# Optimization experiments

Measured on AMD Instinct MI355X. Metric: run time of the kernel, lower is better.

## Reference

```python
import jax, jax.numpy as jnp
import numpy as np

NUM_EDGE_TYPES = 38
NUM_NODE_TYPES = 4
HIDDEN = 64
HOPS = 4
N_NODES = 100_000
N_EDGES = 1_600_000


def setup_inputs() -> dict:
    key = jax.random.key(0)
    ks = jax.random.split(key, 7)
    in_dim = NUM_EDGE_TYPES + 2 * NUM_NODE_TYPES  # 46
    return {
        "edge_index": jax.random.randint(ks[0], (2, N_EDGES), 0, N_NODES),
        "edge_type": jax.random.randint(ks[1], (N_EDGES,), 0, NUM_EDGE_TYPES),
        "node_type": jax.random.randint(ks[2], (N_NODES,), 0, NUM_NODE_TYPES),
        "W1": jax.random.normal(ks[3], (in_dim, HIDDEN), dtype=jnp.float32) * 0.1,
        "b1": jax.random.normal(ks[4], (HIDDEN,), dtype=jnp.float32) * 0.1,
        "W2": jax.random.normal(ks[5], (HIDDEN, 1), dtype=jnp.float32) * 0.1,
        "b2": jax.random.normal(ks[6], (1,), dtype=jnp.float32) * 0.1,
    }


def reference(edge_index, edge_type, node_type, W1, b1, W2, b2):
    src, dst = edge_index[0], edge_index[1]  # PyG: x_j = x[edge_index[0]], aggregate at edge_index[1]
    head_type = node_type[src]
    tail_type = node_type[dst]
    # Linear over concat of three one-hots == sum of three gathered weight rows + bias.
    h = (W1[edge_type]
         + W1[NUM_EDGE_TYPES + head_type]
         + W1[NUM_EDGE_TYPES + NUM_NODE_TYPES + tail_type]
         + b1)                                   # [E, HIDDEN]
    h = jax.nn.gelu(h)
    edge_emb = jax.nn.sigmoid(h @ W2 + b2)       # [E, 1]

    num_nodes = node_type.shape[0]
    aggr = jnp.zeros((num_nodes, 1), dtype=edge_emb.dtype)
    for _ in range(HOPS):
        msg = aggr[src] + edge_emb               # gather + add, [E, 1]
        aggr = jax.ops.segment_sum(msg, dst, num_segments=num_nodes)  # scatter-add
    return aggr
```

## Files before the change

### kernel.cpp

```cpp
#include <hip/hip_runtime.h>

#define NUM_EDGE_TYPES 38
#define NUM_NODE_TYPES 4
#define HIDDEN 64
#define TABLE_SIZE (NUM_EDGE_TYPES * NUM_NODE_TYPES * NUM_NODE_TYPES)
#define SRC_BITS 17
#define SRC_MASK ((1 << SRC_BITS) - 1)
#define BSHIFT 8
#define BNODES 256
#define MAXB 512
#define CHUNK 4096
#define PB 512
#define HB 1024

__global__ void partition_kernel(const int* __restrict__ src, const int* __restrict__ dst,
                                 const int* __restrict__ etype, int* __restrict__ cursor,
                                 int* __restrict__ pack, int E, int nbk, int cap) {
    __shared__ int hist[MAXB];
    __shared__ int locCur[MAXB];
    for (int i = threadIdx.x; i < nbk; i += PB) hist[i] = 0;
    __syncthreads();
    int start = blockIdx.x * CHUNK;
    int end = min(start + CHUNK, E);
    if (end - start == CHUNK) {
        int j = start + threadIdx.x;
        int d[8], s[8], et[8], slot[8];
#pragma unroll
        for (int k = 0; k < 8; ++k) d[k] = dst[j + k * PB];
#pragma unroll
        for (int k = 0; k < 8; ++k) atomicAdd(&hist[d[k] >> BSHIFT], 1);
        __syncthreads();
        for (int i = threadIdx.x; i < nbk; i += PB) {
            int h = hist[i];
            locCur[i] = h ? i * cap + atomicAdd(&cursor[i], h) : 0;
        }
        __syncthreads();
#pragma unroll
        for (int k = 0; k < 8; ++k) s[k] = src[j + k * PB];
#pragma unroll
        for (int k = 0; k < 8; ++k) et[k] = etype[j + k * PB];
#pragma unroll
        for (int k = 0; k < 8; ++k) slot[k] = atomicAdd(&locCur[d[k] >> BSHIFT], 1);
#pragma unroll
        for (int k = 0; k < 8; ++k)
            pack[slot[k]] = (et[k] << (SRC_BITS + 8)) | ((d[k] & (BNODES - 1)) << SRC_BITS) | s[k];
    } else {
        for (int j = start + threadIdx.x; j < end; j += PB)
            atomicAdd(&hist[dst[j] >> BSHIFT], 1);
        __syncthreads();
        for (int i = threadIdx.x; i < nbk; i += PB) {
            int h = hist[i];
            locCur[i] = h ? i * cap + atomicAdd(&cursor[i], h) : 0;
        }
        __syncthreads();
        for (int j = start + threadIdx.x; j < end; j += PB) {
            int d = dst[j];
            int slot = atomicAdd(&locCur[d >> BSHIFT], 1);
            pack[slot] = (etype[j] << (SRC_BITS + 8)) | ((d & (BNODES - 1)) << SRC_BITS) | src[j];
        }
    }
}

__global__ void base_kernel(const int* __restrict__ pack, const int* __restrict__ cursor,
                            const int* __restrict__ ntype,
                            const float* __restrict__ W1, const float* __restrict__ b1,
                            const float* __restrict__ W2, const float* __restrict__ b2,
                            float* __restrict__ base, int N, int cap) {
    __shared__ float bins[BNODES];
    __shared__ float tbl[TABLE_SIZE];
    __shared__ unsigned char ntLoc[BNODES];
    int b = blockIdx.x;
    int node0 = b << BSHIFT;
    if (threadIdx.x < TABLE_SIZE) {
        int i = threadIdx.x;
        int et = i >> 4, ht = (i >> 2) & 3, tt = i & 3;
        const float* r0 = W1 + et * HIDDEN;
        const float* r1 = W1 + (NUM_EDGE_TYPES + ht) * HIDDEN;
        const float* r2 = W1 + (NUM_EDGE_TYPES + NUM_NODE_TYPES + tt) * HIDDEN;
        float acc = b2[0];
#pragma unroll 8
        for (int k = 0; k < HIDDEN; ++k) {
            float h = r0[k] + r1[k] + r2[k] + b1[k];
            float u = 0.7978845608028654f * (h + 0.044715f * h * h * h);
            float g = 0.5f * h * (1.0f + tanhf(u));
            acc += g * W2[k];
        }
        tbl[i] = 1.0f / (1.0f + expf(-acc));
    }
    if (threadIdx.x < BNODES) {
        bins[threadIdx.x] = 0.0f;
        int n = node0 + threadIdx.x;
        ntLoc[threadIdx.x] = (n < N) ? (unsigned char)ntype[n] : 0;
    }
    __syncthreads();
    int st = b * cap;
    int end = st + cursor[b];
    int j = st + threadIdx.x;
    for (; j + 3 * HB < end; j += 4 * HB) {
        int p0 = pack[j], p1 = pack[j + HB], p2 = pack[j + 2 * HB], p3 = pack[j + 3 * HB];
        int n0 = ntype[p0 & SRC_MASK], n1 = ntype[p1 & SRC_MASK];
        int n2 = ntype[p2 & SRC_MASK], n3 = ntype[p3 & SRC_MASK];
        int dl0 = (p0 >> SRC_BITS) & (BNODES - 1), dl1 = (p1 >> SRC_BITS) & (BNODES - 1);
        int dl2 = (p2 >> SRC_BITS) & (BNODES - 1), dl3 = (p3 >> SRC_BITS) & (BNODES - 1);
        atomicAdd(&bins[dl0], tbl[((((unsigned)p0) >> (SRC_BITS + 8)) << 4) | (n0 << 2) | ntLoc[dl0]]);
        atomicAdd(&bins[dl1], tbl[((((unsigned)p1) >> (SRC_BITS + 8)) << 4) | (n1 << 2) | ntLoc[dl1]]);
        atomicAdd(&bins[dl2], tbl[((((unsigned)p2) >> (SRC_BITS + 8)) << 4) | (n2 << 2) | ntLoc[dl2]]);
        atomicAdd(&bins[dl3], tbl[((((unsigned)p3) >> (SRC_BITS + 8)) << 4) | (n3 << 2) | ntLoc[dl3]]);
    }
    for (; j < end; j += HB) {
        int p = pack[j];
        int dl = (p >> SRC_BITS) & (BNODES - 1);
        int idx = ((((unsigned)p) >> (SRC_BITS + 8)) << 4) | (ntype[p & SRC_MASK] << 2) | ntLoc[dl];
        atomicAdd(&bins[dl], tbl[idx]);
    }
    __syncthreads();
    if (threadIdx.x < BNODES) {
        int n = node0 + threadIdx.x;
        if (n < N) base[n] = bins[threadIdx.x];
    }
}

__global__ void hop_kernel(const int* __restrict__ pack, const int* __restrict__ cursor,
                           const float* __restrict__ base, const float* __restrict__ prev,
                           float* __restrict__ out, int N, int cap) {
    __shared__ float bins[BNODES];
    int b = blockIdx.x;
    if (threadIdx.x < BNODES) bins[threadIdx.x] = 0.0f;
    __syncthreads();
    int st = b * cap;
    int end = st + cursor[b];
    int j = st + threadIdx.x;
    for (; j + 3 * HB < end; j += 4 * HB) {
        int p0 = pack[j], p1 = pack[j + HB], p2 = pack[j + 2 * HB], p3 = pack[j + 3 * HB];
        float v0 = prev[p0 & SRC_MASK], v1 = prev[p1 & SRC_MASK];
        float v2 = prev[p2 & SRC_MASK], v3 = prev[p3 & SRC_MASK];
        atomicAdd(&bins[(p0 >> SRC_BITS) & (BNODES - 1)], v0);
        atomicAdd(&bins[(p1 >> SRC_BITS) & (BNODES - 1)], v1);
        atomicAdd(&bins[(p2 >> SRC_BITS) & (BNODES - 1)], v2);
        atomicAdd(&bins[(p3 >> SRC_BITS) & (BNODES - 1)], v3);
    }
    for (; j < end; j += HB) {
        int p = pack[j];
        atomicAdd(&bins[(p >> SRC_BITS) & (BNODES - 1)], prev[p & SRC_MASK]);
    }
    __syncthreads();
    if (threadIdx.x < BNODES) {
        int n = (b << BSHIFT) + threadIdx.x;
        if (n < N) out[n] = base[n] + bins[threadIdx.x];
    }
}

__global__ void table_kernel(const float* __restrict__ W1, const float* __restrict__ b1,
                             const float* __restrict__ W2, const float* __restrict__ b2,
                             float* __restrict__ table) {
    int i = blockIdx.x * blockDim.x + threadIdx.x;
    if (i >= TABLE_SIZE) return;
    int et = i >> 4, ht = (i >> 2) & 3, tt = i & 3;
    const float* r0 = W1 + et * HIDDEN;
    const float* r1 = W1 + (NUM_EDGE_TYPES + ht) * HIDDEN;
    const float* r2 = W1 + (NUM_EDGE_TYPES + NUM_NODE_TYPES + tt) * HIDDEN;
    float acc = b2[0];
#pragma unroll 8
    for (int k = 0; k < HIDDEN; ++k) {
        float h = r0[k] + r1[k] + r2[k] + b1[k];
        float u = 0.7978845608028654f * (h + 0.044715f * h * h * h);
        float g = 0.5f * h * (1.0f + tanhf(u));
        acc += g * W2[k];
    }
    table[i] = 1.0f / (1.0f + expf(-acc));
}

__global__ void edge_base_kernel(const int* __restrict__ src, const int* __restrict__ dst,
                                 const int* __restrict__ etype, const int* __restrict__ ntype,
                                 const float* __restrict__ table, float* __restrict__ base, int E) {
    __shared__ float tbl[TABLE_SIZE];
    for (int i = threadIdx.x; i < TABLE_SIZE; i += blockDim.x) tbl[i] = table[i];
    __syncthreads();
    int e = blockIdx.x * blockDim.x + threadIdx.x;
    if (e >= E) return;
    int s = src[e];
    int d = dst[e];
    int idx = (etype[e] << 4) | (ntype[s] << 2) | ntype[d];
    atomicAdd(base + d, tbl[idx]);
}

__global__ void copy_kernel(const float* __restrict__ in, float* __restrict__ out, int N) {
    int i = blockIdx.x * blockDim.x + threadIdx.x;
    if (i < N) out[i] = in[i];
}

__global__ void edge_hop_kernel(const int* __restrict__ src, const int* __restrict__ dst,
                                const float* __restrict__ prev, float* __restrict__ next, int E) {
    int e = blockIdx.x * blockDim.x + threadIdx.x;
    if (e >= E) return;
    atomicAdd(next + dst[e], prev[src[e]]);
}

extern "C" void kernel_launch(void* const* d_in, const int* in_sizes, int n_in,
                              void* d_out, int out_size, void* d_ws, size_t ws_size,
                              hipStream_t stream) {
    const int* edge_index = (const int*)d_in[0];
    const int* etype      = (const int*)d_in[1];
    const int* ntype      = (const int*)d_in[2];
    const float* W1       = (const float*)d_in[3];
    const float* b1       = (const float*)d_in[4];
    const float* W2       = (const float*)d_in[5];
    const float* b2       = (const float*)d_in[6];

    const int E = in_sizes[1];
    const int N = in_sizes[2];
    const int* src = edge_index;
    const int* dst = edge_index + E;
    float* out = (float*)d_out;

    const int nbk = (N + BNODES - 1) >> BSHIFT;
    const int nChunks = (E + CHUNK - 1) / CHUNK;

    int cap = ((E / (nbk > 0 ? nbk : 1)) * 3 / 2 + 255) & ~255;
    if (cap < 512) cap = 512;
    size_t packElems = (size_t)nbk * cap;

    size_t need = (packElems + MAXB + (size_t)3 * N) * 4 + 256;

    if (ws_size >= need && nbk <= MAXB) {
        int* pack   = (int*)d_ws;
        int* cursor = pack + packElems;
        float* base = (float*)(cursor + MAXB);
        float* bufA = base + N;
        float* bufB = bufA + N;

        hipMemsetAsync(cursor, 0, (size_t)nbk * sizeof(int), stream);

        partition_kernel<<<nChunks, PB, 0, stream>>>(src, dst, etype, cursor, pack, E, nbk, cap);
        base_kernel<<<nbk, HB, 0, stream>>>(pack, cursor, ntype, W1, b1, W2, b2, base, N, cap);
        hop_kernel<<<nbk, HB, 0, stream>>>(pack, cursor, base, base, bufA, N, cap);
        hop_kernel<<<nbk, HB, 0, stream>>>(pack, cursor, base, bufA, bufB, N, cap);
        hop_kernel<<<nbk, HB, 0, stream>>>(pack, cursor, base, bufB, out, N, cap);
    } else {
        float* table = (float*)d_ws;
        float* base  = table + 1024;
        float* bufA  = base + N;
        float* bufB  = bufA + N;
        const int eb = (E + 255) / 256;
        const int nb = (N + 255) / 256;

        hipMemsetAsync(base, 0, (size_t)N * sizeof(float), stream);
        table_kernel<<<(TABLE_SIZE + 255) / 256, 256, 0, stream>>>(W1, b1, W2, b2, table);

        edge_base_kernel<<<eb, 256, 0, stream>>>(src, dst, etype, ntype, table, base, E);
        copy_kernel<<<nb, 256, 0, stream>>>(base, bufA, N);
        edge_hop_kernel<<<eb, 256, 0, stream>>>(src, dst, base, bufA, E);
        copy_kernel<<<nb, 256, 0, stream>>>(base, bufB, N);
        edge_hop_kernel<<<eb, 256, 0, stream>>>(src, dst, bufA, bufB, E);
        copy_kernel<<<nb, 256, 0, stream>>>(base, out, N);
        edge_hop_kernel<<<eb, 256, 0, stream>>>(src, dst, bufB, out, E);
    }
}
```

Baseline: 167.5 us.

## Sort bucket edges by destination into CSR and replace LDS atomics with segmented sums

The base kernel now counting-sorts each bucket's packed edges by local destination node in shared memory, writes the sorted edges back, and stores per-node offsets. The hop kernels then read these CSR segments with four lanes per node and reduce through shuffles, so the shared-memory float atomics on every hop go away. This adds a sort pass and extra writes in the base kernel, and the fast path now requires cap to fit in a fixed shared buffer. Work per node is uneven and each four-lane group does strided small reads, which may hurt coalescing.

```diff
diff --git a/kernel.cpp b/kernel.cpp
--- a/kernel.cpp
+++ b/kernel.cpp
@@ -12,6 +12,7 @@
 #define CHUNK 4096
 #define PB 512
 #define HB 1024
+#define CAPC 6144
 
 __global__ void partition_kernel(const int* __restrict__ src, const int* __restrict__ dst,
                                  const int* __restrict__ etype, int* __restrict__ cursor,
@@ -61,18 +62,26 @@
     }
 }
 
-__global__ void base_kernel(const int* __restrict__ pack, const int* __restrict__ cursor,
-                            const int* __restrict__ ntype,
-                            const float* __restrict__ W1, const float* __restrict__ b1,
-                            const float* __restrict__ W2, const float* __restrict__ b2,
-                            float* __restrict__ base, int N, int cap) {
-    __shared__ float bins[BNODES];
+__global__ void sort_base_kernel(int* __restrict__ pack, const int* __restrict__ cursor,
+                                 const int* __restrict__ ntype,
+                                 const float* __restrict__ W1, const float* __restrict__ b1,
+                                 const float* __restrict__ W2, const float* __restrict__ b2,
+                                 float* __restrict__ base, int* __restrict__ nodeOffG,
+                                 int N, int cap) {
+    __shared__ int sortedL[CAPC];
     __shared__ float tbl[TABLE_SIZE];
+    __shared__ int nodeCnt[BNODES];
+    __shared__ int nodeOff[BNODES + 1];
     __shared__ unsigned char ntLoc[BNODES];
     int b = blockIdx.x;
     int node0 = b << BSHIFT;
-    if (threadIdx.x < TABLE_SIZE) {
-        int i = threadIdx.x;
+    int tid = threadIdx.x;
+    int st = b * cap;
+    int c = cursor[b];
+    c = min(c, cap);
+
+    if (tid < TABLE_SIZE) {
+        int i = tid;
         int et = i >> 4, ht = (i >> 2) & 3, tt = i & 3;
         const float* r0 = W1 + et * HIDDEN;
         const float* r1 = W1 + (NUM_EDGE_TYPES + ht) * HIDDEN;
@@ -87,67 +96,95 @@
         }
         tbl[i] = 1.0f / (1.0f + expf(-acc));
     }
-    if (threadIdx.x < BNODES) {
-        bins[threadIdx.x] = 0.0f;
-        int n = node0 + threadIdx.x;
-        ntLoc[threadIdx.x] = (n < N) ? (unsigned char)ntype[n] : 0;
-    }
-    __syncthreads();
+    if (tid < BNODES) {
+        nodeCnt[tid] = 0;
+        int n = node0 + tid;
+        ntLoc[tid] = (n < N) ? (unsigned char)ntype[n] : 0;
+    }
+    __syncthreads();
+
+    for (int j = tid; j < c; j += HB)
+        atomicAdd(&nodeCnt[(pack[st + j] >> SRC_BITS) & (BNODES - 1)], 1);
+    __syncthreads();
+
+    if (tid < 64) {
+        int lane = tid;
+        int v0 = nodeCnt[lane * 4], v1 = nodeCnt[lane * 4 + 1];
+        int v2 = nodeCnt[lane * 4 + 2], v3 = nodeCnt[lane * 4 + 3];
+        int s = v0 + v1 + v2 + v3;
+        int inc = s;
+        for (int d = 1; d < 64; d <<= 1) {
+            int t = __shfl_up(inc, d, 64);
+            if (lane >= d) inc += t;
+        }
+        int excl = inc - s;
+        nodeOff[lane * 4]     = excl;
+        nodeOff[lane * 4 + 1] = excl + v0;
+        nodeOff[lane * 4 + 2] = excl + v0 + v1;
+        nodeOff[lane * 4 + 3] = excl + v0 + v1 + v2;
+        if (lane == 63) nodeOff[BNODES] = inc;
+    }
+    __syncthreads();
+    if (tid < BNODES) nodeCnt[tid] = 0;
+    __syncthreads();
+
+    for (int j = tid; j < c; j += HB) {
+        int p = pack[st + j];
+        int dl = (p >> SRC_BITS) & (BNODES - 1);
+        int r = atomicAdd(&nodeCnt[dl], 1);
+        sortedL[nodeOff[dl] + r] = p;
+    }
+    __syncthreads();
+
+    for (int j = tid; j < c; j += HB) pack[st + j] = sortedL[j];
+    if (tid < BNODES) nodeOffG[(b << BSHIFT) + tid] = nodeOff[tid];
+
+    int node = tid >> 2, l = tid & 3;
+    int lo = nodeOff[node], hi = nodeOff[node + 1];
+    int nt = ntLoc[node];
+    float s = 0.0f;
+    int j = lo + l;
+    for (; j + 4 < hi; j += 8) {
+        int p0 = sortedL[j], p1 = sortedL[j + 4];
+        int i0 = ((((unsigned)p0) >> (SRC_BITS + 8)) << 4) | (ntype[p0 & SRC_MASK] << 2) | nt;
+        int i1 = ((((unsigned)p1) >> (SRC_BITS + 8)) << 4) | (ntype[p1 & SRC_MASK] << 2) | nt;
+        s += tbl[i0] + tbl[i1];
+    }
+    if (j < hi) {
+        int p = sortedL[j];
+        s += tbl[((((unsigned)p) >> (SRC_BITS + 8)) << 4) | (ntype[p & SRC_MASK] << 2) | nt];
+    }
+    s += __shfl_xor(s, 1, 64);
+    s += __shfl_xor(s, 2, 64);
+    int n = node0 + node;
+    if (l == 0 && n < N) base[n] = s;
+}
+
+__global__ void hop_csr_kernel(const int* __restrict__ pack, const int* __restrict__ nodeOffG,
+                               const int* __restrict__ cursor, const float* __restrict__ base,
+                               const float* __restrict__ prev, float* __restrict__ out,
+                               int N, int cap) {
+    __shared__ int off[BNODES + 1];
+    int b = blockIdx.x;
+    int tid = threadIdx.x;
     int st = b * cap;
-    int end = st + cursor[b];
-    int j = st + threadIdx.x;
-    for (; j + 3 * HB < end; j += 4 * HB) {
-        int p0 = pack[j], p1 = pack[j + HB], p2 = pack[j + 2 * HB], p3 = pack[j + 3 * HB];
-        int n0 = ntype[p0 & SRC_MASK], n1 = ntype[p1 & SRC_MASK];
-        int n2 = ntype[p2 & SRC_MASK], n3 = ntype[p3 & SRC_MASK];
-        int dl0 = (p0 >> SRC_BITS) & (BNODES - 1), dl1 = (p1 >> SRC_BITS) & (BNODES - 1);
-        int dl2 = (p2 >> SRC_BITS) & (BNODES - 1), dl3 = (p3 >> SRC_BITS) & (BNODES - 1);
-        atomicAdd(&bins[dl0], tbl[((((unsigned)p0) >> (SRC_BITS + 8)) << 4) | (n0 << 2) | ntLoc[dl0]]);
-        atomicAdd(&bins[dl1], tbl[((((unsigned)p1) >> (SRC_BITS + 8)) << 4) | (n1 << 2) | ntLoc[dl1]]);
-        atomicAdd(&bins[dl2], tbl[((((unsigned)p2) >> (SRC_BITS + 8)) << 4) | (n2 << 2) | ntLoc[dl2]]);
-        atomicAdd(&bins[dl3], tbl[((((unsigned)p3) >> (SRC_BITS + 8)) << 4) | (n3 << 2) | ntLoc[dl3]]);
-    }
-    for (; j < end; j += HB) {
-        int p = pack[j];
-        int dl = (p >> SRC_BITS) & (BNODES - 1);
-        int idx = ((((unsigned)p) >> (SRC_BITS + 8)) << 4) | (ntype[p & SRC_MASK] << 2) | ntLoc[dl];
-        atomicAdd(&bins[dl], tbl[idx]);
-    }
-    __syncthreads();
-    if (threadIdx.x < BNODES) {
-        int n = node0 + threadIdx.x;
-        if (n < N) base[n] = bins[threadIdx.x];
-    }
-}
-
-__global__ void hop_kernel(const int* __restrict__ pack, const int* __restrict__ cursor,
-                           const float* __restrict__ base, const float* __restrict__ prev,
-                           float* __restrict__ out, int N, int cap) {
-    __shared__ float bins[BNODES];
-    int b = blockIdx.x;
-    if (threadIdx.x < BNODES) bins[threadIdx.x] = 0.0f;
-    __syncthreads();
-    int st = b * cap;
-    int end = st + cursor[b];
-    int j = st + threadIdx.x;
-    for (; j + 3 * HB < end; j += 4 * HB) {
-        int p0 = pack[j], p1 = pack[j + HB], p2 = pack[j + 2 * HB], p3 = pack[j + 3 * HB];
-        float v0 = prev[p0 & SRC_MASK], v1 = prev[p1 & SRC_MASK];
-        float v2 = prev[p2 & SRC_MASK], v3 = prev[p3 & SRC_MASK];
-        atomicAdd(&bins[(p0 >> SRC_BITS) & (BNODES - 1)], v0);
-        atomicAdd(&bins[(p1 >> SRC_BITS) & (BNODES - 1)], v1);
-        atomicAdd(&bins[(p2 >> SRC_BITS) & (BNODES - 1)], v2);
-        atomicAdd(&bins[(p3 >> SRC_BITS) & (BNODES - 1)], v3);
-    }
-    for (; j < end; j += HB) {
-        int p = pack[j];
-        atomicAdd(&bins[(p >> SRC_BITS) & (BNODES - 1)], prev[p & SRC_MASK]);
-    }
-    __syncthreads();
-    if (threadIdx.x < BNODES) {
-        int n = (b << BSHIFT) + threadIdx.x;
-        if (n < N) out[n] = base[n] + bins[threadIdx.x];
-    }
+    if (tid < BNODES) off[tid] = nodeOffG[(b << BSHIFT) + tid];
+    if (tid == 0) off[BNODES] = min(cursor[b], cap);
+    __syncthreads();
+    int node = tid >> 2, l = tid & 3;
+    int lo = off[node], hi = off[node + 1];
+    float s = 0.0f;
+    int j = st + lo + l;
+    int hiG = st + hi;
+    for (; j + 4 < hiG; j += 8) {
+        int p0 = pack[j], p1 = pack[j + 4];
+        s += prev[p0 & SRC_MASK] + prev[p1 & SRC_MASK];
+    }
+    if (j < hiG) s += prev[pack[j] & SRC_MASK];
+    s += __shfl_xor(s, 1, 64);
+    s += __shfl_xor(s, 2, 64);
+    int n = (b << BSHIFT) + node;
+    if (l == 0 && n < N) out[n] = base[n] + s;
 }
 
 __global__ void table_kernel(const float* __restrict__ W1, const float* __restrict__ b1,
@@ -220,22 +257,24 @@
     if (cap < 512) cap = 512;
     size_t packElems = (size_t)nbk * cap;
 
-    size_t need = (packElems + MAXB + (size_t)3 * N) * 4 + 256;
-
-    if (ws_size >= need && nbk <= MAXB) {
-        int* pack   = (int*)d_ws;
-        int* cursor = pack + packElems;
-        float* base = (float*)(cursor + MAXB);
-        float* bufA = base + N;
-        float* bufB = bufA + N;
+    size_t need = (packElems + MAXB + (size_t)nbk * BNODES + (size_t)3 * N) * 4 + 256;
+
+    if (ws_size >= need && nbk <= MAXB && cap <= CAPC) {
+        int* pack     = (int*)d_ws;
+        int* cursor   = pack + packElems;
+        int* nodeOffG = cursor + MAXB;
+        float* base   = (float*)(nodeOffG + (size_t)nbk * BNODES);
+        float* bufA   = base + N;
+        float* bufB   = bufA + N;
 
         hipMemsetAsync(cursor, 0, (size_t)nbk * sizeof(int), stream);
 
         partition_kernel<<<nChunks, PB, 0, stream>>>(src, dst, etype, cursor, pack, E, nbk, cap);
-        base_kernel<<<nbk, HB, 0, stream>>>(pack, cursor, ntype, W1, b1, W2, b2, base, N, cap);
-        hop_kernel<<<nbk, HB, 0, stream>>>(pack, cursor, base, base, bufA, N, cap);
-        hop_kernel<<<nbk, HB, 0, stream>>>(pack, cursor, base, bufA, bufB, N, cap);
-        hop_kernel<<<nbk, HB, 0, stream>>>(pack, cursor, base, bufB, out, N, cap);
+        sort_base_kernel<<<nbk, HB, 0, stream>>>(pack, cursor, ntype, W1, b1, W2, b2,
+                                                 base, nodeOffG, N, cap);
+        hop_csr_kernel<<<nbk, HB, 0, stream>>>(pack, nodeOffG, cursor, base, base, bufA, N, cap);
+        hop_csr_kernel<<<nbk, HB, 0, stream>>>(pack, nodeOffG, cursor, base, bufA, bufB, N, cap);
+        hop_csr_kernel<<<nbk, HB, 0, stream>>>(pack, nodeOffG, cursor, base, bufB, out, N, cap);
     } else {
         float* table = (float*)d_ws;
         float* base  = table + 1024;
```

After: 155.1 us. -7.4%, faster.
